# Optimization experiments

Hardware: AMD Instinct MI355X
Metric: run time of the kernel (lower is better)

Reference implementation:

```python
import jax, jax.numpy as jnp
import numpy as np
from jax import lax

B, T, L = 256, 512, 128


def setup_inputs() -> dict:
    key = jax.random.key(0)
    k1, k2, k3 = jax.random.split(key, 3)
    labels = jax.random.randint(k1, (B, T), 0, L)
    y_true = jax.nn.one_hot(labels, L, dtype=jnp.float32)  # [B,T,L]
    y_pred = jax.random.normal(k2, (B, T, L), dtype=jnp.float32)
    trans = jax.random.normal(k3, (L, L), dtype=jnp.float32) * 0.1
    return {"y_true": y_true, "y_pred": y_pred, "trans": trans}


def reference(y_true, y_pred, trans):
    # ---- log partition via forward algorithm (lax.scan over time) ----
    init = y_pred[:, 0]  # [B,L] initial alpha

    def step(alpha, emit):  # alpha [B,L], emit [B,L]
        # alpha[:, i, None] + trans[i, j] -> logsumexp over previous label i
        new = jax.nn.logsumexp(alpha[:, :, None] + trans[None, :, :], axis=1) + emit
        return new, None

    emits = jnp.swapaxes(y_pred[:, 1:], 0, 1)  # [T-1,B,L]
    final_alpha, _ = lax.scan(step, init, emits)  # [B,L]
    log_norm = jax.nn.logsumexp(final_alpha, axis=1, keepdims=True)  # [B,1]

    # ---- path score (unnormalized log prob of the true path) ----
    point_score = jnp.sum(y_pred * y_true, axis=(1, 2), keepdims=False)[:, None]  # [B,1]
    trans_score = jnp.einsum('bti,btj,ij->b', y_true[:, :-1], y_true[:, 1:], trans)[:, None]  # [B,1]

    return log_norm - (point_score + trans_score)  # [B,1]
```

## Files before the change

kernel.cpp:

```cpp
#include <hip/hip_runtime.h>

typedef float  f32x4 __attribute__((ext_vector_type(4)));
typedef short  s16x8 __attribute__((ext_vector_type(8)));

#define Tt 512
#define Ll 128

#define WS_PT 0
#define WS_TR 256
#define WS_KR 512
#define WS_KB 2304
#define WS_RV 4096
#define WS_BV 233472

__device__ __forceinline__ void bar_lgkm() {
  asm volatile("s_waitcnt lgkmcnt(0)" ::: "memory");
  __builtin_amdgcn_s_barrier();
  asm volatile("" ::: "memory");
}
__device__ __forceinline__ ushort bf16rn(float f) {
  unsigned u = __float_as_uint(f);
  u += 0x7FFFu + ((u >> 16) & 1u);
  return (ushort)(u >> 16);
}
__device__ __forceinline__ float bf16tof(ushort h) {
  return __uint_as_float(((unsigned)h) << 16);
}

__global__ __launch_bounds__(512, 1) void crf_chunk(
    const float* __restrict__ yt_g, const float* __restrict__ yp_g,
    const float* __restrict__ tr_g, float* __restrict__ wsf)
{
  __shared__ __align__(16) ushort ubuf[2][16 * 128];
  __shared__ int lab_s[16][65];

  const int bid = blockIdx.x;
  const int g   = bid / 14, run = bid % 14;
  const bool FWD = (run < 7);
  const int c   = FWD ? run : (run - 6);
  const int b0  = g * 16;
  const int tid = threadIdx.x, wv = tid >> 6, l = tid & 63;
  const int l15 = l & 15, q = l >> 4;
  const int jg  = (wv << 4) | l15;
  const int swA = (l15 & 7) << 4;

  const int t_hi = (c == 7) ? 511 : (c * 64 + 64);
  const int t_lo = c * 64 + 1;
  const int n    = FWD ? 64 : (t_hi - t_lo + 1);

  s16x8 Bf[4];
  #pragma unroll
  for (int kt = 0; kt < 4; ++kt) {
    s16x8 v;
    #pragma unroll
    for (int e = 0; e < 8; ++e) {
      int k = 32 * kt + 8 * q + e;
      float tv = FWD ? tr_g[k * Ll + l15] : tr_g[l15 * Ll + k];
      v[e] = (short)bf16rn(__expf(tv));
    }
    Bf[kt] = v;
  }

  const size_t ypb0 = ((size_t)(b0 + 4 * q + 0) * Tt) * Ll + jg;
  const size_t ypb1 = ((size_t)(b0 + 4 * q + 1) * Tt) * Ll + jg;
  const size_t ypb2 = ((size_t)(b0 + 4 * q + 2) * Tt) * Ll + jg;
  const size_t ypb3 = ((size_t)(b0 + 4 * q + 3) * Tt) * Ll + jg;

  float pt0 = 0.f, pt1 = 0.f, pt2 = 0.f, pt3 = 0.f;
  float K0 = 0.f, K1 = 0.f, K2 = 0.f, K3 = 0.f;
  float res0 = 0.f, res1 = 0.f, res2 = 0.f, res3 = 0.f;

  {
    float iv0, iv1, iv2, iv3;
    if (FWD) {
      if (c == 0) {
        float e0 = yp_g[ypb0], e1 = yp_g[ypb1], e2 = yp_g[ypb2], e3 = yp_g[ypb3];
        float y0 = yt_g[ypb0], y1 = yt_g[ypb1], y2 = yt_g[ypb2], y3 = yt_g[ypb3];
        iv0 = __expf(e0); iv1 = __expf(e1); iv2 = __expf(e2); iv3 = __expf(e3);
        pt0 = e0 * y0; pt1 = e1 * y1; pt2 = e2 * y2; pt3 = e3 * y3;
        if (y0 > .5f) lab_s[4 * q + 0][0] = jg;
        if (y1 > .5f) lab_s[4 * q + 1][0] = jg;
        if (y2 > .5f) lab_s[4 * q + 2][0] = jg;
        if (y3 > .5f) lab_s[4 * q + 3][0] = jg;
      } else { iv0 = iv1 = iv2 = iv3 = 1.f; }
    } else {
      size_t off = (size_t)t_hi * Ll;
      float e0 = yp_g[ypb0 + off], e1 = yp_g[ypb1 + off],
            e2 = yp_g[ypb2 + off], e3 = yp_g[ypb3 + off];
      iv0 = __expf(e0); iv1 = __expf(e1); iv2 = __expf(e2); iv3 = __expf(e3);
      if (c == 7) {
        float y0 = yt_g[ypb0 + off], y1 = yt_g[ypb1 + off],
              y2 = yt_g[ypb2 + off], y3 = yt_g[ypb3 + off];
        pt0 = e0 * y0; pt1 = e1 * y1; pt2 = e2 * y2; pt3 = e3 * y3;
        if (y0 > .5f) lab_s[4 * q + 0][63] = jg;
        if (y1 > .5f) lab_s[4 * q + 1][63] = jg;
        if (y2 > .5f) lab_s[4 * q + 2][63] = jg;
        if (y3 > .5f) lab_s[4 * q + 3][63] = jg;
      }
    }
    char* wb = (char*)ubuf;
    *(ushort*)(wb + (4*q+0)*256 + ((2*jg) ^ (((4*q+0)&7)<<4))) = bf16rn(iv0);
    *(ushort*)(wb + (4*q+1)*256 + ((2*jg) ^ (((4*q+1)&7)<<4))) = bf16rn(iv1);
    *(ushort*)(wb + (4*q+2)*256 + ((2*jg) ^ (((4*q+2)&7)<<4))) = bf16rn(iv2);
    *(ushort*)(wb + (4*q+3)*256 + ((2*jg) ^ (((4*q+3)&7)<<4))) = bf16rn(iv3);
  }

  float PEa0=0,PEa1=0,PEa2=0,PEa3=0, PYa0=0,PYa1=0,PYa2=0,PYa3=0;
  float PEb0=0,PEb1=0,PEb2=0,PEb3=0, PYb0=0,PYb1=0,PYb2=0,PYb3=0;
  {
    int t0s = FWD ? t_lo : (t_hi - 1);
    size_t o = (size_t)t0s * Ll;
    PEa0 = yp_g[ypb0+o]; PEa1 = yp_g[ypb1+o]; PEa2 = yp_g[ypb2+o]; PEa3 = yp_g[ypb3+o];
    if (FWD || c == 7 || 0 >= n - 2) {
      PYa0 = yt_g[ypb0+o]; PYa1 = yt_g[ypb1+o]; PYa2 = yt_g[ypb2+o]; PYa3 = yt_g[ypb3+o];
    }
    int t1s = FWD ? (t_lo + 1) : (t_hi - 2);
    size_t o1 = (size_t)t1s * Ll;
    PEb0 = yp_g[ypb0+o1]; PEb1 = yp_g[ypb1+o1]; PEb2 = yp_g[ypb2+o1]; PEb3 = yp_g[ypb3+o1];
    if (FWD || c == 7 || 1 >= n - 2) {
      PYb0 = yt_g[ypb0+o1]; PYb1 = yt_g[ypb1+o1]; PYb2 = yt_g[ypb2+o1]; PYb3 = yt_g[ypb3+o1];
    }
  }
  bar_lgkm();

#define ITER(K_, PE0,PE1,PE2,PE3, PY0,PY1,PY2,PY3)                            \
  {                                                                           \
    const int cur = (K_) & 1;                                                 \
    const char* abase = (const char*)ubuf + cur * 4096 + l15 * 256;           \
    f32x4 dd = {0.f, 0.f, 0.f, 0.f};                                          \
    _Pragma("unroll")                                                         \
    for (int kt = 0; kt < 4; ++kt) {                                          \
      float4 af = *(const float4*)(abase + ((64 * kt + 16 * q) ^ swA));       \
      dd = __builtin_amdgcn_mfma_f32_16x16x32_bf16(*(const s16x8*)&af,        \
             Bf[kt], dd, 0, 0, 0);                                            \
    }                                                                         \
    const bool last = (K_) == n - 1;                                          \
    const bool ren  = (((K_) & 7) == 7);                                      \
    const int  tsl  = FWD ? (t_lo + (K_)) : (t_hi - (K_) - 1);                \
    const int  li   = tsl - c * 64;                                           \
    const bool doyt = FWD || (c == 7) || (K_) >= n - 2;                       \
    const bool dopt = FWD || ((c == 7) && (K_) <= n - 2);                     \
    float wex0 = __expf(PE0), wex1 = __expf(PE1),                             \
          wex2 = __expf(PE2), wex3 = __expf(PE3);                             \
    if (dopt) { pt0 += PE0*PY0; pt1 += PE1*PY1; pt2 += PE2*PY2; pt3 += PE3*PY3; } \
    if (doyt) {                                                               \
      if (PY0 > .5f) lab_s[4*q+0][li] = jg;                                   \
      if (PY1 > .5f) lab_s[4*q+1][li] = jg;                                   \
      if (PY2 > .5f) lab_s[4*q+2][li] = jg;                                   \
      if (PY3 > .5f) lab_s[4*q+3][li] = jg;                                   \
    }                                                                         \
    float rn0 = 1.f, rn1 = 1.f, rn2 = 1.f, rn3 = 1.f;                         \
    if (ren) {                                                                \
      const char* pb = (const char*)ubuf + cur * 4096;                        \
      float p0 = bf16tof(*(const ushort*)(pb + (4*q+0)*256 + (((4*q+0)&7)<<4))); \
      float p1 = bf16tof(*(const ushort*)(pb + (4*q+1)*256 + (((4*q+1)&7)<<4))); \
      float p2 = bf16tof(*(const ushort*)(pb + (4*q+2)*256 + (((4*q+2)&7)<<4))); \
      float p3 = bf16tof(*(const ushort*)(pb + (4*q+3)*256 + (((4*q+3)&7)<<4))); \
      K0 += __logf(p0); K1 += __logf(p1); K2 += __logf(p2); K3 += __logf(p3); \
      rn0 = 1.f / p0; rn1 = 1.f / p1; rn2 = 1.f / p2; rn3 = 1.f / p3;         \
    }                                                                         \
    float v0 = dd[0], v1 = dd[1], v2 = dd[2], v3 = dd[3];                     \
    if (!(!FWD && last)) { v0 *= wex0; v1 *= wex1; v2 *= wex2; v3 *= wex3; }  \
    if (ren) { v0 *= rn0; v1 *= rn1; v2 *= rn2; v3 *= rn3; }                  \
    if (last) { res0 = v0; res1 = v1; res2 = v2; res3 = v3; }                 \
    else {                                                                    \
      char* wb = (char*)ubuf + (cur ^ 1) * 4096;                              \
      *(ushort*)(wb + (4*q+0)*256 + ((2*jg) ^ (((4*q+0)&7)<<4))) = bf16rn(v0);\
      *(ushort*)(wb + (4*q+1)*256 + ((2*jg) ^ (((4*q+1)&7)<<4))) = bf16rn(v1);\
      *(ushort*)(wb + (4*q+2)*256 + ((2*jg) ^ (((4*q+2)&7)<<4))) = bf16rn(v2);\
      *(ushort*)(wb + (4*q+3)*256 + ((2*jg) ^ (((4*q+3)&7)<<4))) = bf16rn(v3);\
    }                                                                         \
    if ((K_) + 2 < n) {                                                       \
      const int t2 = FWD ? (t_lo + (K_) + 2) : (t_hi - (K_) - 3);             \
      const size_t o2 = (size_t)t2 * Ll;                                      \
      PE0 = yp_g[ypb0+o2]; PE1 = yp_g[ypb1+o2];                               \
      PE2 = yp_g[ypb2+o2]; PE3 = yp_g[ypb3+o2];                               \
      if (FWD || c == 7 || (K_) + 2 >= n - 2) {                               \
        PY0 = yt_g[ypb0+o2]; PY1 = yt_g[ypb1+o2];                             \
        PY2 = yt_g[ypb2+o2]; PY3 = yt_g[ypb3+o2];                             \
      }                                                                       \
    }                                                                         \
    bar_lgkm();                                                               \
  }

  for (int k = 0; k < n; k += 2) {
    ITER(k, PEa0,PEa1,PEa2,PEa3, PYa0,PYa1,PYa2,PYa3)
    if (k + 1 < n) {
      ITER(k + 1, PEb0,PEb1,PEb2,PEb3, PYb0,PYb1,PYb2,PYb3)
    }
  }
#undef ITER

  {
    const int cs = FWD ? c : (c - 1);
    float* rp = wsf + (FWD ? WS_RV : WS_BV);
    rp[((size_t)(b0 + 4*q + 0) * 7 + cs) * 128 + jg] = res0;
    rp[((size_t)(b0 + 4*q + 1) * 7 + cs) * 128 + jg] = res1;
    rp[((size_t)(b0 + 4*q + 2) * 7 + cs) * 128 + jg] = res2;
    rp[((size_t)(b0 + 4*q + 3) * 7 + cs) * 128 + jg] = res3;
    if (wv == 0 && l15 == 0) {
      float* kp = wsf + (FWD ? WS_KR : WS_KB);
      kp[(b0 + 4*q + 0) * 7 + cs] = K0;
      kp[(b0 + 4*q + 1) * 7 + cs] = K1;
      kp[(b0 + 4*q + 2) * 7 + cs] = K2;
      kp[(b0 + 4*q + 3) * 7 + cs] = K3;
    }
  }

  {
    float v;
    v = pt0; v += __shfl_xor(v,1); v += __shfl_xor(v,2); v += __shfl_xor(v,4); v += __shfl_xor(v,8);
    if (l15 == 0) atomicAdd(&wsf[WS_PT + b0 + 4*q + 0], v);
    v = pt1; v += __shfl_xor(v,1); v += __shfl_xor(v,2); v += __shfl_xor(v,4); v += __shfl_xor(v,8);
    if (l15 == 0) atomicAdd(&wsf[WS_PT + b0 + 4*q + 1], v);
    v = pt2; v += __shfl_xor(v,1); v += __shfl_xor(v,2); v += __shfl_xor(v,4); v += __shfl_xor(v,8);
    if (l15 == 0) atomicAdd(&wsf[WS_PT + b0 + 4*q + 2], v);
    v = pt3; v += __shfl_xor(v,1); v += __shfl_xor(v,2); v += __shfl_xor(v,4); v += __shfl_xor(v,8);
    if (l15 == 0) atomicAdd(&wsf[WS_PT + b0 + 4*q + 3], v);
  }

  {
    int pbase, npair;
    if (FWD) { pbase = (c == 0) ? 0 : 1; npair = (c == 0) ? 64 : 63; }
    else     { pbase = 0; npair = (c == 7) ? 63 : 1; }
    const int bl = tid >> 5, l32 = tid & 31;
    float trl = 0.f;
    for (int p = pbase + l32; p < pbase + npair; p += 32)
      trl += tr_g[lab_s[bl][p] * Ll + lab_s[bl][p + 1]];
    trl += __shfl_xor(trl, 16); trl += __shfl_xor(trl, 8);
    trl += __shfl_xor(trl, 4);  trl += __shfl_xor(trl, 2);
    trl += __shfl_xor(trl, 1);
    if (l32 == 0) atomicAdd(&wsf[WS_TR + b0 + bl], trl);
  }
}

__global__ __launch_bounds__(64) void crf_stitch(
    const float* __restrict__ wsf, float* __restrict__ out)
{
  const int b = blockIdx.x, j = threadIdx.x;
  const float* RV = wsf + WS_RV + (size_t)b * 7 * 128;
  const float* BV = wsf + WS_BV + (size_t)b * 7 * 128;
  const float* Kr = wsf + WS_KR + b * 7;
  const float* Kb = wsf + WS_KB + b * 7;
  float lz;
  {
    float d = RV[j] * BV[j] + RV[j + 64] * BV[j + 64];
    #pragma unroll
    for (int o = 32; o; o >>= 1) d += __shfl_xor(d, o);
    lz = __logf(d) + Kr[0] + Kb[0];
  }
  #pragma unroll
  for (int cc = 1; cc < 7; ++cc) {
    float d = RV[cc*128 + j] * BV[cc*128 + j] + RV[cc*128 + j + 64] * BV[cc*128 + j + 64];
    float s = RV[cc*128 + j] + RV[cc*128 + j + 64];
    #pragma unroll
    for (int o = 32; o; o >>= 1) { d += __shfl_xor(d, o); s += __shfl_xor(s, o); }
    lz += __logf(d) - __logf(s) + Kb[cc];
  }
  if (j == 0) out[b] = lz - wsf[WS_PT + b] - wsf[WS_TR + b];
}

extern "C" void kernel_launch(void* const* d_in, const int* in_sizes, int n_in,
                              void* d_out, int out_size, void* d_ws, size_t ws_size,
                              hipStream_t stream) {
  const float* y_true = (const float*)d_in[0];
  const float* y_pred = (const float*)d_in[1];
  const float* trans  = (const float*)d_in[2];
  float* out = (float*)d_out;
  float* wsf = (float*)d_ws;
  hipMemsetAsync(d_ws, 0, 2048, stream);
  crf_chunk<<<dim3(224), dim3(512), 0, stream>>>(y_true, y_pred, trans, wsf);
  crf_stitch<<<dim3(256), dim3(64), 0, stream>>>(wsf, out);
}
```

Baseline: 78.08 us.

## Split time into 16 chunks and move path scoring to dedicated blocks

The forward/backward chunked recurrence now uses 16 chunks of 32 steps instead of 8 of 64, so 480 recurrence blocks run shorter serial chains in place of 224 longer ones. The point score and transition score of the true path move into 256 separate per-batch blocks that read y_pred and y_true with float4 loads and reduce in shared memory. This drops the y_true loads, label bookkeeping, atomics and memset from the recurrence blocks. The trade-off is more blocks than CUs with one block per CU, a larger workspace, and a stitch step that must combine more chunks.

Result: faster. 65.79 us (-15.7%).

```diff
diff --git a/kernel.cpp b/kernel.cpp
--- a/kernel.cpp
+++ b/kernel.cpp
@@ -5,13 +5,18 @@
 
 #define Tt 512
 #define Ll 128
+#define CH 16
+#define CL 32
+#define NR 15
+#define RUNS 30
+#define NSCORE 256
 
 #define WS_PT 0
 #define WS_TR 256
 #define WS_KR 512
-#define WS_KB 2304
-#define WS_RV 4096
-#define WS_BV 233472
+#define WS_KB (512 + 256*NR)
+#define WS_RV (512 + 2*256*NR)
+#define WS_BV (WS_RV + 256*NR*128)
 
 __device__ __forceinline__ void bar_lgkm() {
   asm volatile("s_waitcnt lgkmcnt(0)" ::: "memory");
@@ -32,21 +37,54 @@
     const float* __restrict__ tr_g, float* __restrict__ wsf)
 {
   __shared__ __align__(16) ushort ubuf[2][16 * 128];
-  __shared__ int lab_s[16][65];
-
-  const int bid = blockIdx.x;
-  const int g   = bid / 14, run = bid % 14;
-  const bool FWD = (run < 7);
-  const int c   = FWD ? run : (run - 6);
-  const int b0  = g * 16;
+  __shared__ int   lab_s[Tt];
+  __shared__ float redp[8], redt[8];
+
   const int tid = threadIdx.x, wv = tid >> 6, l = tid & 63;
-  const int l15 = l & 15, q = l >> 4;
-  const int jg  = (wv << 4) | l15;
-  const int swA = (l15 & 7) << 4;
-
-  const int t_hi = (c == 7) ? 511 : (c * 64 + 64);
-  const int t_lo = c * 64 + 1;
-  const int n    = FWD ? 64 : (t_hi - t_lo + 1);
+
+  if (blockIdx.x < NSCORE) {
+    const int b = blockIdx.x;
+    const float4* yp4 = (const float4*)(yp_g + (size_t)b * Tt * Ll);
+    const float4* yt4 = (const float4*)(yt_g + (size_t)b * Tt * Ll);
+    float pt = 0.f;
+    #pragma unroll 4
+    for (int i = 0; i < 32; ++i) {
+      int f = tid + i * 512;
+      float4 a = yp4[f], y = yt4[f];
+      pt += a.x * y.x + a.y * y.y + a.z * y.z + a.w * y.w;
+      int t = f >> 5, jb = (f & 31) << 2;
+      if (y.x > .5f) lab_s[t] = jb;
+      if (y.y > .5f) lab_s[t] = jb + 1;
+      if (y.z > .5f) lab_s[t] = jb + 2;
+      if (y.w > .5f) lab_s[t] = jb + 3;
+    }
+    __syncthreads();
+    float trl = (tid < Tt - 1) ? tr_g[lab_s[tid] * Ll + lab_s[tid + 1]] : 0.f;
+    #pragma unroll
+    for (int o = 32; o; o >>= 1) { pt += __shfl_xor(pt, o); trl += __shfl_xor(trl, o); }
+    if (l == 0) { redp[wv] = pt; redt[wv] = trl; }
+    __syncthreads();
+    if (tid == 0) {
+      float sp = 0.f, st = 0.f;
+      #pragma unroll
+      for (int k2 = 0; k2 < 8; ++k2) { sp += redp[k2]; st += redt[k2]; }
+      wsf[WS_PT + b] = sp; wsf[WS_TR + b] = st;
+    }
+    return;
+  }
+
+  const int bid2 = blockIdx.x - NSCORE;
+  const int g    = bid2 / RUNS, run = bid2 % RUNS;
+  const bool FWD = (run < NR);
+  const int c    = FWD ? run : (run - NR + 1);
+  const int b0   = g * 16;
+  const int l15  = l & 15, q = l >> 4;
+  const int jg   = (wv << 4) | l15;
+  const int swA  = (l15 & 7) << 4;
+
+  const int t_hi = (c == CH - 1) ? (Tt - 1) : (c * CL + CL);
+  const int t_lo = c * CL + 1;
+  const int n    = FWD ? CL : (t_hi - t_lo + 1);
 
   s16x8 Bf[4];
   #pragma unroll
@@ -66,7 +104,6 @@
   const size_t ypb2 = ((size_t)(b0 + 4 * q + 2) * Tt) * Ll + jg;
   const size_t ypb3 = ((size_t)(b0 + 4 * q + 3) * Tt) * Ll + jg;
 
-  float pt0 = 0.f, pt1 = 0.f, pt2 = 0.f, pt3 = 0.f;
   float K0 = 0.f, K1 = 0.f, K2 = 0.f, K3 = 0.f;
   float res0 = 0.f, res1 = 0.f, res2 = 0.f, res3 = 0.f;
 
@@ -74,29 +111,13 @@
     float iv0, iv1, iv2, iv3;
     if (FWD) {
       if (c == 0) {
-        float e0 = yp_g[ypb0], e1 = yp_g[ypb1], e2 = yp_g[ypb2], e3 = yp_g[ypb3];
-        float y0 = yt_g[ypb0], y1 = yt_g[ypb1], y2 = yt_g[ypb2], y3 = yt_g[ypb3];
-        iv0 = __expf(e0); iv1 = __expf(e1); iv2 = __expf(e2); iv3 = __expf(e3);
-        pt0 = e0 * y0; pt1 = e1 * y1; pt2 = e2 * y2; pt3 = e3 * y3;
-        if (y0 > .5f) lab_s[4 * q + 0][0] = jg;
-        if (y1 > .5f) lab_s[4 * q + 1][0] = jg;
-        if (y2 > .5f) lab_s[4 * q + 2][0] = jg;
-        if (y3 > .5f) lab_s[4 * q + 3][0] = jg;
+        iv0 = __expf(yp_g[ypb0]); iv1 = __expf(yp_g[ypb1]);
+        iv2 = __expf(yp_g[ypb2]); iv3 = __expf(yp_g[ypb3]);
       } else { iv0 = iv1 = iv2 = iv3 = 1.f; }
     } else {
       size_t off = (size_t)t_hi * Ll;
-      float e0 = yp_g[ypb0 + off], e1 = yp_g[ypb1 + off],
-            e2 = yp_g[ypb2 + off], e3 = yp_g[ypb3 + off];
-      iv0 = __expf(e0); iv1 = __expf(e1); iv2 = __expf(e2); iv3 = __expf(e3);
-      if (c == 7) {
-        float y0 = yt_g[ypb0 + off], y1 = yt_g[ypb1 + off],
-              y2 = yt_g[ypb2 + off], y3 = yt_g[ypb3 + off];
-        pt0 = e0 * y0; pt1 = e1 * y1; pt2 = e2 * y2; pt3 = e3 * y3;
-        if (y0 > .5f) lab_s[4 * q + 0][63] = jg;
-        if (y1 > .5f) lab_s[4 * q + 1][63] = jg;
-        if (y2 > .5f) lab_s[4 * q + 2][63] = jg;
-        if (y3 > .5f) lab_s[4 * q + 3][63] = jg;
-      }
+      iv0 = __expf(yp_g[ypb0 + off]); iv1 = __expf(yp_g[ypb1 + off]);
+      iv2 = __expf(yp_g[ypb2 + off]); iv3 = __expf(yp_g[ypb3 + off]);
     }
     char* wb = (char*)ubuf;
     *(ushort*)(wb + (4*q+0)*256 + ((2*jg) ^ (((4*q+0)&7)<<4))) = bf16rn(iv0);
@@ -105,25 +126,16 @@
     *(ushort*)(wb + (4*q+3)*256 + ((2*jg) ^ (((4*q+3)&7)<<4))) = bf16rn(iv3);
   }
 
-  float PEa0=0,PEa1=0,PEa2=0,PEa3=0, PYa0=0,PYa1=0,PYa2=0,PYa3=0;
-  float PEb0=0,PEb1=0,PEb2=0,PEb3=0, PYb0=0,PYb1=0,PYb2=0,PYb3=0;
-  {
-    int t0s = FWD ? t_lo : (t_hi - 1);
-    size_t o = (size_t)t0s * Ll;
-    PEa0 = yp_g[ypb0+o]; PEa1 = yp_g[ypb1+o]; PEa2 = yp_g[ypb2+o]; PEa3 = yp_g[ypb3+o];
-    if (FWD || c == 7 || 0 >= n - 2) {
-      PYa0 = yt_g[ypb0+o]; PYa1 = yt_g[ypb1+o]; PYa2 = yt_g[ypb2+o]; PYa3 = yt_g[ypb3+o];
-    }
-    int t1s = FWD ? (t_lo + 1) : (t_hi - 2);
-    size_t o1 = (size_t)t1s * Ll;
+  float PEa0, PEa1, PEa2, PEa3, PEb0, PEb1, PEb2, PEb3;
+  {
+    size_t o0 = (size_t)(FWD ? t_lo : (t_hi - 1)) * Ll;
+    PEa0 = yp_g[ypb0+o0]; PEa1 = yp_g[ypb1+o0]; PEa2 = yp_g[ypb2+o0]; PEa3 = yp_g[ypb3+o0];
+    size_t o1 = (size_t)(FWD ? (t_lo + 1) : (t_hi - 2)) * Ll;
     PEb0 = yp_g[ypb0+o1]; PEb1 = yp_g[ypb1+o1]; PEb2 = yp_g[ypb2+o1]; PEb3 = yp_g[ypb3+o1];
-    if (FWD || c == 7 || 1 >= n - 2) {
-      PYb0 = yt_g[ypb0+o1]; PYb1 = yt_g[ypb1+o1]; PYb2 = yt_g[ypb2+o1]; PYb3 = yt_g[ypb3+o1];
-    }
   }
   bar_lgkm();
 
-#define ITER(K_, PE0,PE1,PE2,PE3, PY0,PY1,PY2,PY3)                            \
+#define ITER(K_, PE0,PE1,PE2,PE3)                                             \
   {                                                                           \
     const int cur = (K_) & 1;                                                 \
     const char* abase = (const char*)ubuf + cur * 4096 + l15 * 256;           \
@@ -136,19 +148,8 @@
     }                                                                         \
     const bool last = (K_) == n - 1;                                          \
     const bool ren  = (((K_) & 7) == 7);                                      \
-    const int  tsl  = FWD ? (t_lo + (K_)) : (t_hi - (K_) - 1);                \
-    const int  li   = tsl - c * 64;                                           \
-    const bool doyt = FWD || (c == 7) || (K_) >= n - 2;                       \
-    const bool dopt = FWD || ((c == 7) && (K_) <= n - 2);                     \
     float wex0 = __expf(PE0), wex1 = __expf(PE1),                             \
           wex2 = __expf(PE2), wex3 = __expf(PE3);                             \
-    if (dopt) { pt0 += PE0*PY0; pt1 += PE1*PY1; pt2 += PE2*PY2; pt3 += PE3*PY3; } \
-    if (doyt) {                                                               \
-      if (PY0 > .5f) lab_s[4*q+0][li] = jg;                                   \
-      if (PY1 > .5f) lab_s[4*q+1][li] = jg;                                   \
-      if (PY2 > .5f) lab_s[4*q+2][li] = jg;                                   \
-      if (PY3 > .5f) lab_s[4*q+3][li] = jg;                                   \
-    }                                                                         \
     float rn0 = 1.f, rn1 = 1.f, rn2 = 1.f, rn3 = 1.f;                         \
     if (ren) {                                                                \
       const char* pb = (const char*)ubuf + cur * 4096;                        \
@@ -171,22 +172,18 @@
       *(ushort*)(wb + (4*q+3)*256 + ((2*jg) ^ (((4*q+3)&7)<<4))) = bf16rn(v3);\
     }                                                                         \
     if ((K_) + 2 < n) {                                                       \
-      const int t2 = FWD ? (t_lo + (K_) + 2) : (t_hi - (K_) - 3);             \
-      const size_t o2 = (size_t)t2 * Ll;                                      \
+      const size_t o2 = (size_t)(FWD ? (t_lo + (K_) + 2)                      \
+                                     : (t_hi - (K_) - 3)) * Ll;               \
       PE0 = yp_g[ypb0+o2]; PE1 = yp_g[ypb1+o2];                               \
       PE2 = yp_g[ypb2+o2]; PE3 = yp_g[ypb3+o2];                               \
-      if (FWD || c == 7 || (K_) + 2 >= n - 2) {                               \
-        PY0 = yt_g[ypb0+o2]; PY1 = yt_g[ypb1+o2];                             \
-        PY2 = yt_g[ypb2+o2]; PY3 = yt_g[ypb3+o2];                             \
-      }                                                                       \
     }                                                                         \
     bar_lgkm();                                                               \
   }
 
   for (int k = 0; k < n; k += 2) {
-    ITER(k, PEa0,PEa1,PEa2,PEa3, PYa0,PYa1,PYa2,PYa3)
+    ITER(k, PEa0, PEa1, PEa2, PEa3)
     if (k + 1 < n) {
-      ITER(k + 1, PEb0,PEb1,PEb2,PEb3, PYb0,PYb1,PYb2,PYb3)
+      ITER(k + 1, PEb0, PEb1, PEb2, PEb3)
     }
   }
 #undef ITER
@@ -194,43 +191,17 @@
   {
     const int cs = FWD ? c : (c - 1);
     float* rp = wsf + (FWD ? WS_RV : WS_BV);
-    rp[((size_t)(b0 + 4*q + 0) * 7 + cs) * 128 + jg] = res0;
-    rp[((size_t)(b0 + 4*q + 1) * 7 + cs) * 128 + jg] = res1;
-    rp[((size_t)(b0 + 4*q + 2) * 7 + cs) * 128 + jg] = res2;
-    rp[((size_t)(b0 + 4*q + 3) * 7 + cs) * 128 + jg] = res3;
+    rp[((size_t)(b0 + 4*q + 0) * NR + cs) * 128 + jg] = res0;
+    rp[((size_t)(b0 + 4*q + 1) * NR + cs) * 128 + jg] = res1;
+    rp[((size_t)(b0 + 4*q + 2) * NR + cs) * 128 + jg] = res2;
+    rp[((size_t)(b0 + 4*q + 3) * NR + cs) * 128 + jg] = res3;
     if (wv == 0 && l15 == 0) {
       float* kp = wsf + (FWD ? WS_KR : WS_KB);
-      kp[(b0 + 4*q + 0) * 7 + cs] = K0;
-      kp[(b0 + 4*q + 1) * 7 + cs] = K1;
-      kp[(b0 + 4*q + 2) * 7 + cs] = K2;
-      kp[(b0 + 4*q + 3) * 7 + cs] = K3;
-    }
-  }
-
-  {
-    float v;
-    v = pt0; v += __shfl_xor(v,1); v += __shfl_xor(v,2); v += __shfl_xor(v,4); v += __shfl_xor(v,8);
-    if (l15 == 0) atomicAdd(&wsf[WS_PT + b0 + 4*q + 0], v);
-    v = pt1; v += __shfl_xor(v,1); v += __shfl_xor(v,2); v += __shfl_xor(v,4); v += __shfl_xor(v,8);
-    if (l15 == 0) atomicAdd(&wsf[WS_PT + b0 + 4*q + 1], v);
-    v = pt2; v += __shfl_xor(v,1); v += __shfl_xor(v,2); v += __shfl_xor(v,4); v += __shfl_xor(v,8);
-    if (l15 == 0) atomicAdd(&wsf[WS_PT + b0 + 4*q + 2], v);
-    v = pt3; v += __shfl_xor(v,1); v += __shfl_xor(v,2); v += __shfl_xor(v,4); v += __shfl_xor(v,8);
-    if (l15 == 0) atomicAdd(&wsf[WS_PT + b0 + 4*q + 3], v);
-  }
-
-  {
-    int pbase, npair;
-    if (FWD) { pbase = (c == 0) ? 0 : 1; npair = (c == 0) ? 64 : 63; }
-    else     { pbase = 0; npair = (c == 7) ? 63 : 1; }
-    const int bl = tid >> 5, l32 = tid & 31;
-    float trl = 0.f;
-    for (int p = pbase + l32; p < pbase + npair; p += 32)
-      trl += tr_g[lab_s[bl][p] * Ll + lab_s[bl][p + 1]];
-    trl += __shfl_xor(trl, 16); trl += __shfl_xor(trl, 8);
-    trl += __shfl_xor(trl, 4);  trl += __shfl_xor(trl, 2);
-    trl += __shfl_xor(trl, 1);
-    if (l32 == 0) atomicAdd(&wsf[WS_TR + b0 + bl], trl);
+      kp[(b0 + 4*q + 0) * NR + cs] = K0;
+      kp[(b0 + 4*q + 1) * NR + cs] = K1;
+      kp[(b0 + 4*q + 2) * NR + cs] = K2;
+      kp[(b0 + 4*q + 3) * NR + cs] = K3;
+    }
   }
 }
 
@@ -238,10 +209,10 @@
     const float* __restrict__ wsf, float* __restrict__ out)
 {
   const int b = blockIdx.x, j = threadIdx.x;
-  const float* RV = wsf + WS_RV + (size_t)b * 7 * 128;
-  const float* BV = wsf + WS_BV + (size_t)b * 7 * 128;
-  const float* Kr = wsf + WS_KR + b * 7;
-  const float* Kb = wsf + WS_KB + b * 7;
+  const float* RV = wsf + WS_RV + (size_t)b * NR * 128;
+  const float* BV = wsf + WS_BV + (size_t)b * NR * 128;
+  const float* Kr = wsf + WS_KR + b * NR;
+  const float* Kb = wsf + WS_KB + b * NR;
   float lz;
   {
     float d = RV[j] * BV[j] + RV[j + 64] * BV[j + 64];
@@ -250,7 +221,7 @@
     lz = __logf(d) + Kr[0] + Kb[0];
   }
   #pragma unroll
-  for (int cc = 1; cc < 7; ++cc) {
+  for (int cc = 1; cc < NR; ++cc) {
     float d = RV[cc*128 + j] * BV[cc*128 + j] + RV[cc*128 + j + 64] * BV[cc*128 + j + 64];
     float s = RV[cc*128 + j] + RV[cc*128 + j + 64];
     #pragma unroll
@@ -268,7 +239,6 @@
   const float* trans  = (const float*)d_in[2];
   float* out = (float*)d_out;
   float* wsf = (float*)d_ws;
-  hipMemsetAsync(d_ws, 0, 2048, stream);
-  crf_chunk<<<dim3(224), dim3(512), 0, stream>>>(y_true, y_pred, trans, wsf);
+  crf_chunk<<<dim3(NSCORE + 16 * RUNS), dim3(512), 0, stream>>>(y_true, y_pred, trans, wsf);
   crf_stitch<<<dim3(256), dim3(64), 0, stream>>>(wsf, out);
 }
```
